# Optimization experiments

Measured on AMD Instinct MI355X. Metric: run time of the kernel, lower is better.

The kernel has to match this reference:

```python
import jax, jax.numpy as jnp
import numpy as np

N, E, D, H = 100000, 1000000, 128, 8
DH = D // H
SCALE = 1.0 / np.sqrt(DH)


def setup_inputs() -> dict:
    key = jax.random.key(0)
    ks = jax.random.split(key, 12)
    inp = {
        "x": jax.random.normal(ks[0], (N, D), jnp.float32),
        "edge_index": jax.random.randint(ks[1], (2, E), 0, N, dtype=jnp.int64),
        "a": jnp.array(0.25, jnp.float32),  # shared PReLU slope
    }
    names = ["Wq1", "Wk1", "Wv1", "Ws1", "Wq2", "Wk2", "Wv2", "Ws2"]
    for i, n in enumerate(names):
        # kaiming_normal_: std = sqrt(2 / fan_in)
        inp[n] = jax.random.normal(ks[2 + i], (D, D), jnp.float32) * np.sqrt(2.0 / D)
        inp["b" + n[1:]] = jnp.zeros((D,), jnp.float32)
    return inp


def prelu(x, a):
    return jnp.where(x >= 0, x, a * x)


def transformer_conv(x, src, dst, Wq, bq, Wk, bk, Wv, bv, Ws, bs):
    # PyG TransformerConv: query from target (dst), key/value from source (src),
    # scatter-softmax over incoming edges of each dst node, root skip via lin_skip.
    q = (x @ Wq + bq).reshape(N, H, DH)
    k = (x @ Wk + bk).reshape(N, H, DH)
    v = (x @ Wv + bv).reshape(N, H, DH)
    score = jnp.einsum("ehd,ehd->eh", q[dst], k[src]) * SCALE  # [E, H]
    m = jax.lax.stop_gradient(jax.ops.segment_max(score, dst, num_segments=N))  # [N, H]
    e = jnp.exp(score - m[dst])
    s = jax.ops.segment_sum(e, dst, num_segments=N)  # [N, H]
    alpha = e / s[dst]  # scatter-softmax, [E, H]
    agg = jax.ops.segment_sum(alpha[..., None] * v[src], dst, num_segments=N)  # [N, H, DH]
    return agg.reshape(N, D) + x @ Ws + bs


def reference(x, edge_index, a,
              Wq1, bq1, Wk1, bk1, Wv1, bv1, Ws1, bs1,
              Wq2, bq2, Wk2, bk2, Wv2, bv2, Ws2, bs2):
    src, dst = edge_index[0], edge_index[1]
    h = transformer_conv(x, src, dst, Wq1, bq1, Wk1, bk1, Wv1, bv1, Ws1, bs1)
    h = prelu(h, a)
    h = transformer_conv(h, src, dst, Wq2, bq2, Wk2, bk2, Wv2, bv2, Ws2, bs2)
    h = h + x
    return prelu(h, a)
```

## Files before the change

### kernel.cpp

```cpp
#include <hip/hip_runtime.h>
#include <hip/hip_bf16.h>
#include <math.h>

#define D 128
#define SCALE 0.25f
#define NEG_BIG (-1e30f)

typedef __attribute__((ext_vector_type(8))) short bf16x8;
typedef __attribute__((ext_vector_type(4))) float f32x4;

__device__ inline __hip_bfloat162 pack2(float a, float b) {
    __hip_bfloat162 h;
    h.x = __float2bfloat16(a);
    h.y = __float2bfloat16(b);
    return h;
}

__device__ inline int detect_is64(const int* __restrict__ ei) {
    int lane = threadIdx.x & 63;
    int v = ei[2 * lane + 1];
    unsigned long long b = __ballot(v != 0);
    return b == 0ULL;
}

struct PackArgs { const float* w[8]; };

__global__ __launch_bounds__(256) void prep(
    PackArgs pa, __hip_bfloat16* __restrict__ WtP,
    const float* __restrict__ x, __hip_bfloat16* __restrict__ xb, int n4,
    const int* __restrict__ ei, int E, int* __restrict__ deg, int gE)
{
    int b = blockIdx.x;
    int tid = threadIdx.x;
    if (b < gE) {
        int is64 = detect_is64(ei);
        int e = b * 256 + tid;
        if (e < E) {
            int d = is64 ? ei[2 * E + 2 * e] : ei[E + e];
            atomicAdd(&deg[d], 1);
        }
    } else if (b < gE + 8) {
        int w = b - gE;
        const float* W = pa.w[w];
        __hip_bfloat16* dst = WtP + (size_t)w * 128 * 128;
        for (int idx = tid; idx < 128 * 128; idx += 256) {
            int c = idx & 127, k = idx >> 7;
            dst[(size_t)c * 128 + k] = __float2bfloat16(W[(size_t)k * 128 + c]);
        }
    } else {
        int i = (b - gE - 8) * 256 + tid;
        if (i < n4) {
            float4 v = ((const float4*)x)[i];
            ((__hip_bfloat162*)xb)[2 * i]     = pack2(v.x, v.y);
            ((__hip_bfloat162*)xb)[2 * i + 1] = pack2(v.z, v.w);
        }
    }
}

__global__ __launch_bounds__(1024) void scan_blocks(const int* __restrict__ deg,
                                                    int* __restrict__ row_ptr,
                                                    int* __restrict__ bsum, int Nn) {
    __shared__ int buf[1024];
    int tid = threadIdx.x;
    int i = blockIdx.x * 1024 + tid;
    int v = (i < Nn) ? deg[i] : 0;
    buf[tid] = v;
    __syncthreads();
    for (int off = 1; off < 1024; off <<= 1) {
        int t = (tid >= off) ? buf[tid - off] : 0;
        __syncthreads();
        buf[tid] += t;
        __syncthreads();
    }
    if (i < Nn) row_ptr[i] = buf[tid] - v;
    if (tid == 1023) bsum[blockIdx.x] = buf[1023];
}

__global__ __launch_bounds__(1024) void scan_bsum(int* __restrict__ bsum,
                                                  int* __restrict__ boff,
                                                  int NB, int* __restrict__ row_ptr, int Nn) {
    __shared__ int buf[1024];
    int tid = threadIdx.x;
    int v = (tid < NB) ? bsum[tid] : 0;
    buf[tid] = v;
    __syncthreads();
    for (int off = 1; off < 1024; off <<= 1) {
        int t = (tid >= off) ? buf[tid - off] : 0;
        __syncthreads();
        buf[tid] += t;
        __syncthreads();
    }
    if (tid < NB) boff[tid] = buf[tid] - v;
    if (tid == 0) row_ptr[Nn] = buf[NB - 1];
}

__global__ void add_offsets(int* __restrict__ row_ptr, int* __restrict__ cursor,
                            const int* __restrict__ boff, int Nn) {
    int i = blockIdx.x * blockDim.x + threadIdx.x;
    if (i < Nn) {
        int r = row_ptr[i] + boff[i >> 10];
        row_ptr[i] = r;
        cursor[i] = r;
    }
}

#define TSTR 136

__device__ __forceinline__ void gemm_body(
    int bx, __hip_bfloat16* bufA, __hip_bfloat16* bufB,
    const __hip_bfloat16* __restrict__ A, const __hip_bfloat16* __restrict__ Wt,
    const float* __restrict__ bq, const float* __restrict__ bk,
    const float* __restrict__ bv, const float* __restrict__ bs,
    __hip_bfloat16* __restrict__ qb, __hip_bfloat16* __restrict__ kv,
    __hip_bfloat16* __restrict__ skipb, int M)
{
    const int tid = threadIdx.x;
    const int w = tid >> 6, lane = tid & 63;
    const int wr = w >> 1, wc = w & 1;
    const int blk0 = bx * 64;
    const int rowBase = blk0 + wr * 32;
    const int l16 = lane & 15;
    const int quad = lane >> 4;

    bf16x8 xfrag[2][4];
    #pragma unroll
    for (int i = 0; i < 2; ++i) {
        int r = rowBase + i * 16 + l16;
        if (r >= M) r = M - 1;
        #pragma unroll
        for (int kb = 0; kb < 4; ++kb)
            xfrag[i][kb] = *(const bf16x8*)(A + (size_t)r * D + kb * 32 + quad * 8);
    }

    const float* biases[4] = {bq, bk, bv, bs};

    for (int cb = 0; cb < 4; ++cb) {
        const __hip_bfloat16* Wblk = Wt + (size_t)cb * 128 * 128;
        f32x4 acc[2][4];
        #pragma unroll
        for (int i = 0; i < 2; i++)
            #pragma unroll
            for (int jt = 0; jt < 4; jt++) acc[i][jt] = (f32x4){0.f, 0.f, 0.f, 0.f};

        #pragma unroll
        for (int kb = 0; kb < 4; ++kb) {
            const int k0 = kb * 32 + quad * 8;
            #pragma unroll
            for (int jt = 0; jt < 4; ++jt) {
                int c = wc * 64 + jt * 16 + l16;
                bf16x8 wfrag = *(const bf16x8*)(Wblk + (size_t)c * D + k0);
                acc[0][jt] = __builtin_amdgcn_mfma_f32_16x16x32_bf16(wfrag, xfrag[0][kb], acc[0][jt], 0, 0, 0);
                acc[1][jt] = __builtin_amdgcn_mfma_f32_16x16x32_bf16(wfrag, xfrag[1][kb], acc[1][jt], 0, 0, 0);
            }
        }

        __hip_bfloat16* dst = (cb == 2) ? bufB : bufA;
        const float* bias = biases[cb];
        #pragma unroll
        for (int jt = 0; jt < 4; ++jt) {
            int c0 = wc * 64 + jt * 16 + quad * 4;
            float4 bb = *(const float4*)(bias + c0);
            #pragma unroll
            for (int i = 0; i < 2; ++i) {
                int lrow = wr * 32 + i * 16 + l16;
                f32x4 vv = acc[i][jt];
                __hip_bfloat162 h0 = pack2(vv[0] + bb.x, vv[1] + bb.y);
                __hip_bfloat162 h1 = pack2(vv[2] + bb.z, vv[3] + bb.w);
                float2 st; st.x = *(float*)&h0; st.y = *(float*)&h1;
                *(float2*)(&dst[lrow * TSTR + c0]) = st;
            }
        }

        if (cb == 1) continue;

        __syncthreads();

        if (cb == 0 || cb == 3) {
            __hip_bfloat16* gout = (cb == 0) ? qb : skipb;
            #pragma unroll
            for (int it = 0; it < 4; ++it) {
                int lrow = it * 16 + (tid >> 4);
                int grow = blk0 + lrow;
                if (grow < M) {
                    float4 vv = *(const float4*)(&bufA[lrow * TSTR + (tid & 15) * 8]);
                    *(float4*)(gout + (size_t)grow * D + (tid & 15) * 8) = vv;
                }
            }
        } else {
            #pragma unroll
            for (int it = 0; it < 8; ++it) {
                int lrow = it * 8 + (tid >> 5);
                int grow = blk0 + lrow;
                int g = tid & 31;
                if (grow < M) {
                    float2 kk = *(const float2*)(&bufA[lrow * TSTR + g * 4]);
                    float2 vv = *(const float2*)(&bufB[lrow * TSTR + g * 4]);
                    float4 o; o.x = kk.x; o.y = kk.y; o.z = vv.x; o.w = vv.y;
                    *(float4*)(kv + (size_t)grow * 256 + g * 8) = o;
                }
            }
        }
        __syncthreads();
    }
}

__global__ __launch_bounds__(256) void gemm_mfma(
    const __hip_bfloat16* __restrict__ A, const __hip_bfloat16* __restrict__ Wt,
    const float* __restrict__ bq, const float* __restrict__ bk,
    const float* __restrict__ bv, const float* __restrict__ bs,
    __hip_bfloat16* __restrict__ qb, __hip_bfloat16* __restrict__ kv,
    __hip_bfloat16* __restrict__ skipb, int M)
{
    __shared__ __hip_bfloat16 bufA[64 * TSTR];
    __shared__ __hip_bfloat16 bufB[64 * TSTR];
    gemm_body(blockIdx.x, bufA, bufB, A, Wt, bq, bk, bv, bs, qb, kv, skipb, M);
}

__global__ __launch_bounds__(256) void gemm_scatter(
    const __hip_bfloat16* __restrict__ A, const __hip_bfloat16* __restrict__ Wt,
    const float* __restrict__ bq, const float* __restrict__ bk,
    const float* __restrict__ bv, const float* __restrict__ bs,
    __hip_bfloat16* __restrict__ qb, __hip_bfloat16* __restrict__ kv,
    __hip_bfloat16* __restrict__ skipb, int M,
    const int* __restrict__ ei, int E,
    int* __restrict__ cursor, int* __restrict__ srcs, int gE)
{
    __shared__ __hip_bfloat16 bufA[64 * TSTR];
    __shared__ __hip_bfloat16 bufB[64 * TSTR];
    if (blockIdx.x < gE) {
        int is64 = detect_is64(ei);
        int e = blockIdx.x * 256 + threadIdx.x;
        if (e < E) {
            int s = is64 ? ei[2 * e]         : ei[e];
            int d = is64 ? ei[2 * E + 2 * e] : ei[E + e];
            int pos = atomicAdd(&cursor[d], 1);
            srcs[pos] = s;
        }
    } else {
        gemm_body(blockIdx.x - gE, bufA, bufB, A, Wt, bq, bk, bv, bs, qb, kv, skipb, M);
    }
}

__device__ inline void store4(float* base, size_t off, float o0, float o1, float o2, float o3) {
    *(float4*)(base + off) = make_float4(o0, o1, o2, o3);
}
__device__ inline void store4(__hip_bfloat16* base, size_t off, float o0, float o1, float o2, float o3) {
    __hip_bfloat162 h0 = pack2(o0, o1), h1 = pack2(o2, o3);
    float2 st; st.x = *(float*)&h0; st.y = *(float*)&h1;
    *(float2*)(base + off) = st;
}

template <typename OutT>
__global__ __launch_bounds__(256) void attn_agg(
    const __hip_bfloat16* __restrict__ qb, const __hip_bfloat16* __restrict__ kv,
    const int* __restrict__ row_ptr, const int* __restrict__ srcs,
    const __hip_bfloat16* __restrict__ skip, const __hip_bfloat16* __restrict__ residb,
    const float* __restrict__ a_ptr, OutT* __restrict__ out, int Nn) {
    int tid = threadIdx.x;
    int lane = tid & 63;
    int half = lane >> 5;
    int lh = lane & 31;
    int n = blockIdx.x * 8 + (tid >> 6) * 2 + half;
    bool valid = (n < Nn);
    int nc = valid ? n : (Nn - 1);
    const float a = a_ptr[0];

    float2 qraw = *(const float2*)(qb + (size_t)nc * D + 4 * lh);
    __hip_bfloat162 q01 = *(__hip_bfloat162*)&qraw.x;
    __hip_bfloat162 q23 = *(__hip_bfloat162*)&qraw.y;
    float q0 = __bfloat162float(q01.x) * SCALE, q1 = __bfloat162float(q01.y) * SCALE;
    float q2 = __bfloat162float(q23.x) * SCALE, q3 = __bfloat162float(q23.y) * SCALE;

    float m = NEG_BIG, s = 0.f, A0 = 0.f, A1 = 0.f, A2 = 0.f, A3 = 0.f;

    int beg = row_ptr[nc];
    int end = valid ? row_ptr[nc + 1] : beg;
    int cnt = end - beg;
    int cmax = max(cnt, __shfl_xor(cnt, 32));
    int last = (cnt > 0) ? (end - 1) : 0;

    const float4* kvp4 = (const float4*)kv;

    for (int t = 0; t < cmax; t += 8) {
        float4 f[8];
        float sc[8];
        #pragma unroll
        for (int i = 0; i < 8; ++i) {
            int j = beg + t + i;
            int jj = (j < last) ? j : last;
            int src = srcs[jj];
            f[i] = kvp4[(size_t)src * 32 + lh];
        }
        #pragma unroll
        for (int i = 0; i < 8; ++i) {
            __hip_bfloat162 k01 = *(__hip_bfloat162*)&f[i].x;
            __hip_bfloat162 k23 = *(__hip_bfloat162*)&f[i].y;
            float p = q0 * __bfloat162float(k01.x) + q1 * __bfloat162float(k01.y)
                    + q2 * __bfloat162float(k23.x) + q3 * __bfloat162float(k23.y);
            p += __shfl_xor(p, 1);
            p += __shfl_xor(p, 2);
            sc[i] = (t + i < cnt) ? p : NEG_BIG;
        }
        float nm = m;
        #pragma unroll
        for (int i = 0; i < 8; ++i) nm = fmaxf(nm, sc[i]);
        float corr = __expf(m - nm);
        A0 *= corr; A1 *= corr; A2 *= corr; A3 *= corr; s *= corr;
        #pragma unroll
        for (int i = 0; i < 8; ++i) {
            float wgt = __expf(sc[i] - nm);
            __hip_bfloat162 v01 = *(__hip_bfloat162*)&f[i].z;
            __hip_bfloat162 v23 = *(__hip_bfloat162*)&f[i].w;
            A0 += wgt * __bfloat162float(v01.x);
            A1 += wgt * __bfloat162float(v01.y);
            A2 += wgt * __bfloat162float(v23.x);
            A3 += wgt * __bfloat162float(v23.y);
            s += wgt;
        }
        m = nm;
    }

    if (!valid) return;
    float inv = (cnt > 0) ? 1.f / s : 0.f;
    float2 skr = *(const float2*)(skip + (size_t)n * D + 4 * lh);
    __hip_bfloat162 s01 = *(__hip_bfloat162*)&skr.x;
    __hip_bfloat162 s23 = *(__hip_bfloat162*)&skr.y;
    float o0 = A0 * inv + __bfloat162float(s01.x);
    float o1 = A1 * inv + __bfloat162float(s01.y);
    float o2 = A2 * inv + __bfloat162float(s23.x);
    float o3 = A3 * inv + __bfloat162float(s23.y);
    if (residb) {
        float2 rr = *(const float2*)(residb + (size_t)n * D + 4 * lh);
        __hip_bfloat162 r01 = *(__hip_bfloat162*)&rr.x;
        __hip_bfloat162 r23 = *(__hip_bfloat162*)&rr.y;
        o0 += __bfloat162float(r01.x);
        o1 += __bfloat162float(r01.y);
        o2 += __bfloat162float(r23.x);
        o3 += __bfloat162float(r23.y);
    }
    o0 = (o0 >= 0.f) ? o0 : a * o0;
    o1 = (o1 >= 0.f) ? o1 : a * o1;
    o2 = (o2 >= 0.f) ? o2 : a * o2;
    o3 = (o3 >= 0.f) ? o3 : a * o3;
    store4(out, (size_t)n * D + 4 * lh, o0, o1, o2, o3);
}

extern "C" void kernel_launch(void* const* d_in, const int* in_sizes, int n_in,
                              void* d_out, int out_size, void* d_ws, size_t ws_size,
                              hipStream_t stream) {
    const float* x  = (const float*)d_in[0];
    const int*   ei = (const int*)d_in[1];
    const float* a  = (const float*)d_in[2];
    const float* Wq1 = (const float*)d_in[3];  const float* bq1 = (const float*)d_in[4];
    const float* Wk1 = (const float*)d_in[5];  const float* bk1 = (const float*)d_in[6];
    const float* Wv1 = (const float*)d_in[7];  const float* bv1 = (const float*)d_in[8];
    const float* Ws1 = (const float*)d_in[9];  const float* bs1 = (const float*)d_in[10];
    const float* Wq2 = (const float*)d_in[11]; const float* bq2 = (const float*)d_in[12];
    const float* Wk2 = (const float*)d_in[13]; const float* bk2 = (const float*)d_in[14];
    const float* Wv2 = (const float*)d_in[15]; const float* bv2 = (const float*)d_in[16];
    const float* Ws2 = (const float*)d_in[17]; const float* bs2 = (const float*)d_in[18];

    const int N = in_sizes[0] / D;
    const int E = in_sizes[1] / 2;
    const size_t NF = (size_t)N * D;

    char* wp = (char*)d_ws;
    __hip_bfloat16* xb    = (__hip_bfloat16*)wp; wp += NF * 2;
    __hip_bfloat16* h1b   = (__hip_bfloat16*)wp; wp += NF * 2;
    __hip_bfloat16* qb    = (__hip_bfloat16*)wp; wp += NF * 2;
    __hip_bfloat16* kv    = (__hip_bfloat16*)wp; wp += NF * 4;
    __hip_bfloat16* skipb = (__hip_bfloat16*)wp; wp += NF * 2;
    __hip_bfloat16* WtP   = (__hip_bfloat16*)wp; wp += 2 * 512 * 128 * 2;
    int* deg     = (int*)wp;  wp += (size_t)N * 4;
    int* row_ptr = (int*)wp;  wp += (size_t)(N + 64) * 4;
    int* cursor  = (int*)wp;  wp += (size_t)N * 4;
    int* bsum    = (int*)wp;  wp += 1024 * 4;
    int* boff    = (int*)wp;  wp += 1024 * 4;
    int* srcs    = (int*)wp;  wp += (size_t)E * 4;
    float* out   = (float*)d_out;

    const int TB = 256;
    int gN = (N + TB - 1) / TB;
    int gE = (E + TB - 1) / TB;
    int NB = (N + 1023) / 1024;
    int gGemm = (N + 63) / 64;
    int gAttn = (N + 7) / 8;
    int n4 = (int)(NF / 4);
    int gCvt = (n4 + TB - 1) / TB;

    PackArgs pa;
    pa.w[0] = Wq1; pa.w[1] = Wk1; pa.w[2] = Wv1; pa.w[3] = Ws1;
    pa.w[4] = Wq2; pa.w[5] = Wk2; pa.w[6] = Wv2; pa.w[7] = Ws2;

    hipMemsetAsync(deg, 0, (size_t)N * 4, stream);
    hipLaunchKernelGGL(prep, dim3(gE + 8 + gCvt), dim3(TB), 0, stream,
                       pa, WtP, x, xb, n4, ei, E, deg, gE);

    hipLaunchKernelGGL(scan_blocks, dim3(NB), dim3(1024), 0, stream, deg, row_ptr, bsum, N);
    hipLaunchKernelGGL(scan_bsum, dim3(1), dim3(1024), 0, stream, bsum, boff, NB, row_ptr, N);
    hipLaunchKernelGGL(add_offsets, dim3(gN), dim3(TB), 0, stream, row_ptr, cursor, boff, N);

    hipLaunchKernelGGL(gemm_scatter, dim3(gE + gGemm), dim3(TB), 0, stream,
                       xb, WtP, bq1, bk1, bv1, bs1, qb, kv, skipb, N,
                       ei, E, cursor, srcs, gE);
    hipLaunchKernelGGL(attn_agg<__hip_bfloat16>, dim3(gAttn), dim3(TB), 0, stream,
                       qb, kv, row_ptr, srcs, skipb, (const __hip_bfloat16*)nullptr, a, h1b, N);

    hipLaunchKernelGGL(gemm_mfma, dim3(gGemm), dim3(TB), 0, stream,
                       h1b, WtP + 512 * 128, bq2, bk2, bv2, bs2, qb, kv, skipb, N);
    hipLaunchKernelGGL(attn_agg<float>, dim3(gAttn), dim3(TB), 0, stream,
                       qb, kv, row_ptr, srcs, skipb, xb, a, out, N);
}
```

Baseline: 567.7 us.

## Replace CSR build with fixed-slot adjacency plus overflow list

Replaces the degree-count, three-kernel prefix scan and separate scatter pass with a single atomic pass. That pass writes each edge's source into a fixed 32-slot per-node bucket and spills any excess into a global overflow list. The attention kernel reads the slot buckets directly and scans the whole overflow list only when some node in the wave exceeds 32 edges. This removes four launches and the scatter phase, at the cost of a larger memset (N*32 ints) and sparser slot reads. It also risks a slow linear overflow scan if degrees exceed 32.

```diff
diff --git a/kernel.cpp b/kernel.cpp
--- a/kernel.cpp
+++ b/kernel.cpp
@@ -5,6 +5,7 @@
 #define D 128
 #define SCALE 0.25f
 #define NEG_BIG (-1e30f)
+#define SLOTS 32
 
 typedef __attribute__((ext_vector_type(8))) short bf16x8;
 typedef __attribute__((ext_vector_type(4))) float f32x4;
@@ -28,7 +29,9 @@
 __global__ __launch_bounds__(256) void prep(
     PackArgs pa, __hip_bfloat16* __restrict__ WtP,
     const float* __restrict__ x, __hip_bfloat16* __restrict__ xb, int n4,
-    const int* __restrict__ ei, int E, int* __restrict__ deg, int gE)
+    const int* __restrict__ ei, int E,
+    int* __restrict__ deg, int* __restrict__ slots,
+    unsigned long long* __restrict__ ovf, int* __restrict__ ovfcnt, int gE)
 {
     int b = blockIdx.x;
     int tid = threadIdx.x;
@@ -36,8 +39,15 @@
         int is64 = detect_is64(ei);
         int e = b * 256 + tid;
         if (e < E) {
+            int s = is64 ? ei[2 * e]         : ei[e];
             int d = is64 ? ei[2 * E + 2 * e] : ei[E + e];
-            atomicAdd(&deg[d], 1);
+            int pos = atomicAdd(&deg[d], 1);
+            if (pos < SLOTS) {
+                slots[d * SLOTS + pos] = s;
+            } else {
+                int op = atomicAdd(ovfcnt, 1);
+                ovf[op] = ((unsigned long long)(unsigned)d << 32) | (unsigned)s;
+            }
         }
     } else if (b < gE + 8) {
         int w = b - gE;
@@ -57,67 +67,22 @@
     }
 }
 
-__global__ __launch_bounds__(1024) void scan_blocks(const int* __restrict__ deg,
-                                                    int* __restrict__ row_ptr,
-                                                    int* __restrict__ bsum, int Nn) {
-    __shared__ int buf[1024];
-    int tid = threadIdx.x;
-    int i = blockIdx.x * 1024 + tid;
-    int v = (i < Nn) ? deg[i] : 0;
-    buf[tid] = v;
-    __syncthreads();
-    for (int off = 1; off < 1024; off <<= 1) {
-        int t = (tid >= off) ? buf[tid - off] : 0;
-        __syncthreads();
-        buf[tid] += t;
-        __syncthreads();
-    }
-    if (i < Nn) row_ptr[i] = buf[tid] - v;
-    if (tid == 1023) bsum[blockIdx.x] = buf[1023];
-}
-
-__global__ __launch_bounds__(1024) void scan_bsum(int* __restrict__ bsum,
-                                                  int* __restrict__ boff,
-                                                  int NB, int* __restrict__ row_ptr, int Nn) {
-    __shared__ int buf[1024];
-    int tid = threadIdx.x;
-    int v = (tid < NB) ? bsum[tid] : 0;
-    buf[tid] = v;
-    __syncthreads();
-    for (int off = 1; off < 1024; off <<= 1) {
-        int t = (tid >= off) ? buf[tid - off] : 0;
-        __syncthreads();
-        buf[tid] += t;
-        __syncthreads();
-    }
-    if (tid < NB) boff[tid] = buf[tid] - v;
-    if (tid == 0) row_ptr[Nn] = buf[NB - 1];
-}
-
-__global__ void add_offsets(int* __restrict__ row_ptr, int* __restrict__ cursor,
-                            const int* __restrict__ boff, int Nn) {
-    int i = blockIdx.x * blockDim.x + threadIdx.x;
-    if (i < Nn) {
-        int r = row_ptr[i] + boff[i >> 10];
-        row_ptr[i] = r;
-        cursor[i] = r;
-    }
-}
-
 #define TSTR 136
 
-__device__ __forceinline__ void gemm_body(
-    int bx, __hip_bfloat16* bufA, __hip_bfloat16* bufB,
+__global__ __launch_bounds__(256) void gemm_mfma(
     const __hip_bfloat16* __restrict__ A, const __hip_bfloat16* __restrict__ Wt,
     const float* __restrict__ bq, const float* __restrict__ bk,
     const float* __restrict__ bv, const float* __restrict__ bs,
     __hip_bfloat16* __restrict__ qb, __hip_bfloat16* __restrict__ kv,
     __hip_bfloat16* __restrict__ skipb, int M)
 {
+    __shared__ __hip_bfloat16 bufA[64 * TSTR];
+    __shared__ __hip_bfloat16 bufB[64 * TSTR];
+
     const int tid = threadIdx.x;
     const int w = tid >> 6, lane = tid & 63;
     const int wr = w >> 1, wc = w & 1;
-    const int blk0 = bx * 64;
+    const int blk0 = blockIdx.x * 64;
     const int rowBase = blk0 + wr * 32;
     const int l16 = lane & 15;
     const int quad = lane >> 4;
@@ -204,43 +169,6 @@
     }
 }
 
-__global__ __launch_bounds__(256) void gemm_mfma(
-    const __hip_bfloat16* __restrict__ A, const __hip_bfloat16* __restrict__ Wt,
-    const float* __restrict__ bq, const float* __restrict__ bk,
-    const float* __restrict__ bv, const float* __restrict__ bs,
-    __hip_bfloat16* __restrict__ qb, __hip_bfloat16* __restrict__ kv,
-    __hip_bfloat16* __restrict__ skipb, int M)
-{
-    __shared__ __hip_bfloat16 bufA[64 * TSTR];
-    __shared__ __hip_bfloat16 bufB[64 * TSTR];
-    gemm_body(blockIdx.x, bufA, bufB, A, Wt, bq, bk, bv, bs, qb, kv, skipb, M);
-}
-
-__global__ __launch_bounds__(256) void gemm_scatter(
-    const __hip_bfloat16* __restrict__ A, const __hip_bfloat16* __restrict__ Wt,
-    const float* __restrict__ bq, const float* __restrict__ bk,
-    const float* __restrict__ bv, const float* __restrict__ bs,
-    __hip_bfloat16* __restrict__ qb, __hip_bfloat16* __restrict__ kv,
-    __hip_bfloat16* __restrict__ skipb, int M,
-    const int* __restrict__ ei, int E,
-    int* __restrict__ cursor, int* __restrict__ srcs, int gE)
-{
-    __shared__ __hip_bfloat16 bufA[64 * TSTR];
-    __shared__ __hip_bfloat16 bufB[64 * TSTR];
-    if (blockIdx.x < gE) {
-        int is64 = detect_is64(ei);
-        int e = blockIdx.x * 256 + threadIdx.x;
-        if (e < E) {
-            int s = is64 ? ei[2 * e]         : ei[e];
-            int d = is64 ? ei[2 * E + 2 * e] : ei[E + e];
-            int pos = atomicAdd(&cursor[d], 1);
-            srcs[pos] = s;
-        }
-    } else {
-        gemm_body(blockIdx.x - gE, bufA, bufB, A, Wt, bq, bk, bv, bs, qb, kv, skipb, M);
-    }
-}
-
 __device__ inline void store4(float* base, size_t off, float o0, float o1, float o2, float o3) {
     *(float4*)(base + off) = make_float4(o0, o1, o2, o3);
 }
@@ -253,7 +181,8 @@
 template <typename OutT>
 __global__ __launch_bounds__(256) void attn_agg(
     const __hip_bfloat16* __restrict__ qb, const __hip_bfloat16* __restrict__ kv,
-    const int* __restrict__ row_ptr, const int* __restrict__ srcs,
+    const int* __restrict__ deg, const int* __restrict__ slots,
+    const unsigned long long* __restrict__ ovf, const int* __restrict__ ovfcnt,
     const __hip_bfloat16* __restrict__ skip, const __hip_bfloat16* __restrict__ residb,
     const float* __restrict__ a_ptr, OutT* __restrict__ out, int Nn) {
     int tid = threadIdx.x;
@@ -273,11 +202,10 @@
 
     float m = NEG_BIG, s = 0.f, A0 = 0.f, A1 = 0.f, A2 = 0.f, A3 = 0.f;
 
-    int beg = row_ptr[nc];
-    int end = valid ? row_ptr[nc + 1] : beg;
-    int cnt = end - beg;
-    int cmax = max(cnt, __shfl_xor(cnt, 32));
-    int last = (cnt > 0) ? (end - 1) : 0;
+    int cnt = valid ? deg[nc] : 0;
+    int cmain = min(cnt, SLOTS);
+    int cmax = max(cmain, __shfl_xor(cmain, 32));
+    int beg = nc * SLOTS;
 
     const float4* kvp4 = (const float4*)kv;
 
@@ -286,9 +214,7 @@
         float sc[8];
         #pragma unroll
         for (int i = 0; i < 8; ++i) {
-            int j = beg + t + i;
-            int jj = (j < last) ? j : last;
-            int src = srcs[jj];
+            int src = slots[beg + t + i];
             f[i] = kvp4[(size_t)src * 32 + lh];
         }
         #pragma unroll
@@ -299,7 +225,7 @@
                     + q2 * __bfloat162float(k23.x) + q3 * __bfloat162float(k23.y);
             p += __shfl_xor(p, 1);
             p += __shfl_xor(p, 2);
-            sc[i] = (t + i < cnt) ? p : NEG_BIG;
+            sc[i] = (t + i < cmain) ? p : NEG_BIG;
         }
         float nm = m;
         #pragma unroll
@@ -318,6 +244,35 @@
             s += wgt;
         }
         m = nm;
+    }
+
+    if (__any(cnt > SLOTS)) {
+        int oc = *ovfcnt;
+        for (int i = 0; i < oc; ++i) {
+            unsigned long long e = ovf[i];
+            int dd = (int)(e >> 32);
+            int ss = (int)(e & 0xffffffffULL);
+            bool take = (dd == nc) && (cnt > SLOTS) && valid;
+            float4 fo = kvp4[(size_t)ss * 32 + lh];
+            __hip_bfloat162 k01 = *(__hip_bfloat162*)&fo.x;
+            __hip_bfloat162 k23 = *(__hip_bfloat162*)&fo.y;
+            float p = q0 * __bfloat162float(k01.x) + q1 * __bfloat162float(k01.y)
+                    + q2 * __bfloat162float(k23.x) + q3 * __bfloat162float(k23.y);
+            p += __shfl_xor(p, 1);
+            p += __shfl_xor(p, 2);
+            float sce = take ? p : NEG_BIG;
+            float nm = fmaxf(m, sce);
+            float corr = __expf(m - nm);
+            float wgt = take ? __expf(sce - nm) : 0.f;
+            __hip_bfloat162 v01 = *(__hip_bfloat162*)&fo.z;
+            __hip_bfloat162 v23 = *(__hip_bfloat162*)&fo.w;
+            A0 = A0 * corr + wgt * __bfloat162float(v01.x);
+            A1 = A1 * corr + wgt * __bfloat162float(v01.y);
+            A2 = A2 * corr + wgt * __bfloat162float(v23.x);
+            A3 = A3 * corr + wgt * __bfloat162float(v23.y);
+            s = s * corr + wgt;
+            m = nm;
+        }
     }
 
     if (!valid) return;
@@ -371,18 +326,15 @@
     __hip_bfloat16* kv    = (__hip_bfloat16*)wp; wp += NF * 4;
     __hip_bfloat16* skipb = (__hip_bfloat16*)wp; wp += NF * 2;
     __hip_bfloat16* WtP   = (__hip_bfloat16*)wp; wp += 2 * 512 * 128 * 2;
-    int* deg     = (int*)wp;  wp += (size_t)N * 4;
-    int* row_ptr = (int*)wp;  wp += (size_t)(N + 64) * 4;
-    int* cursor  = (int*)wp;  wp += (size_t)N * 4;
-    int* bsum    = (int*)wp;  wp += 1024 * 4;
-    int* boff    = (int*)wp;  wp += 1024 * 4;
-    int* srcs    = (int*)wp;  wp += (size_t)E * 4;
-    float* out   = (float*)d_out;
+    int* deg    = (int*)wp;                wp += (size_t)N * 4;
+    int* ovfcnt = (int*)wp;                wp += 64;
+    int* slots  = (int*)wp;                wp += (size_t)N * SLOTS * 4;
+    size_t zbytes = (size_t)N * 4 + 64 + (size_t)N * SLOTS * 4;
+    unsigned long long* ovf = (unsigned long long*)wp; wp += (size_t)E * 8;
+    float* out = (float*)d_out;
 
     const int TB = 256;
-    int gN = (N + TB - 1) / TB;
     int gE = (E + TB - 1) / TB;
-    int NB = (N + 1023) / 1024;
     int gGemm = (N + 63) / 64;
     int gAttn = (N + 7) / 8;
     int n4 = (int)(NF / 4);
@@ -392,22 +344,18 @@
     pa.w[0] = Wq1; pa.w[1] = Wk1; pa.w[2] = Wv1; pa.w[3] = Ws1;
     pa.w[4] = Wq2; pa.w[5] = Wk2; pa.w[6] = Wv2; pa.w[7] = Ws2;
 
-    hipMemsetAsync(deg, 0, (size_t)N * 4, stream);
+    hipMemsetAsync(deg, 0, zbytes, stream);
     hipLaunchKernelGGL(prep, dim3(gE + 8 + gCvt), dim3(TB), 0, stream,
-                       pa, WtP, x, xb, n4, ei, E, deg, gE);
-
-    hipLaunchKernelGGL(scan_blocks, dim3(NB), dim3(1024), 0, stream, deg, row_ptr, bsum, N);
-    hipLaunchKernelGGL(scan_bsum, dim3(1), dim3(1024), 0, stream, bsum, boff, NB, row_ptr, N);
-    hipLaunchKernelGGL(add_offsets, dim3(gN), dim3(TB), 0, stream, row_ptr, cursor, boff, N);
-
-    hipLaunchKernelGGL(gemm_scatter, dim3(gE + gGemm), dim3(TB), 0, stream,
-                       xb, WtP, bq1, bk1, bv1, bs1, qb, kv, skipb, N,
-                       ei, E, cursor, srcs, gE);
+                       pa, WtP, x, xb, n4, ei, E, deg, slots, ovf, ovfcnt, gE);
+
+    hipLaunchKernelGGL(gemm_mfma, dim3(gGemm), dim3(TB), 0, stream,
+                       xb, WtP, bq1, bk1, bv1, bs1, qb, kv, skipb, N);
     hipLaunchKernelGGL(attn_agg<__hip_bfloat16>, dim3(gAttn), dim3(TB), 0, stream,
-                       qb, kv, row_ptr, srcs, skipb, (const __hip_bfloat16*)nullptr, a, h1b, N);
+                       qb, kv, deg, slots, ovf, ovfcnt, skipb,
+                       (const __hip_bfloat16*)nullptr, a, h1b, N);
 
     hipLaunchKernelGGL(gemm_mfma, dim3(gGemm), dim3(TB), 0, stream,
                        h1b, WtP + 512 * 128, bq2, bk2, bv2, bs2, qb, kv, skipb, N);
     hipLaunchKernelGGL(attn_agg<float>, dim3(gAttn), dim3(TB), 0, stream,
-                       qb, kv, row_ptr, srcs, skipb, xb, a, out, N);
-}
+                       qb, kv, deg, slots, ovf, ovfcnt, skipb, xb, a, out, N);
+}
```

After: 524.8 us. 7.6% less time.
